# Optimization experiments

Measured on AMD Instinct MI355X. Metric: run time of the kernel, lower is better.

## Reference

```python
import jax, jax.numpy as jnp
import numpy as np

B, S, D, H = 2, 2048, 1024, 16
DK = D // H  # 64
THETA = 10000.0


def setup_inputs() -> dict:
    key = jax.random.key(0)
    ks = jax.random.split(key, 5)
    scale = 1.0 / np.sqrt(D)
    return {
        "x": jax.random.normal(ks[0], (B, S, D), dtype=jnp.float32),
        "Wq": jax.random.normal(ks[1], (D, D), dtype=jnp.float32) * scale,
        "Wk": jax.random.normal(ks[2], (D, D), dtype=jnp.float32) * scale,
        "Wv": jax.random.normal(ks[3], (D, D), dtype=jnp.float32) * scale,
        "Wo": jax.random.normal(ks[4], (D, D), dtype=jnp.float32) * scale,
    }


def _rope(t):
    # t: (B, H, S, DK); interleaved-pair rotary embedding with positions 0..S-1
    s = t.shape[-2]
    inv_freq = 1.0 / (THETA ** (jnp.arange(0, DK, 2, dtype=jnp.float32) / DK))  # (DK/2,)
    ang = jnp.arange(s, dtype=jnp.float32)[:, None] * inv_freq[None, :]  # (S, DK/2)
    cos, sin = jnp.cos(ang), jnp.sin(ang)
    x1 = t[..., 0::2]
    x2 = t[..., 1::2]
    r1 = x1 * cos - x2 * sin
    r2 = x1 * sin + x2 * cos
    return jnp.stack([r1, r2], axis=-1).reshape(t.shape)


def reference(x, Wq, Wk, Wv, Wo):
    # Projections (Linear: y = x @ W^T), split heads -> (B, H, S, DK)
    def proj(W):
        y = jnp.einsum('bsd,ed->bse', x, W)
        return y.reshape(B, S, H, DK).transpose(0, 2, 1, 3)

    Q = _rope(proj(Wq))
    K = _rope(proj(Wk))
    V = proj(Wv)

    scores = jnp.einsum('bhqd,bhkd->bhqk', Q, K)
    scores = jnp.clip(scores, -80.0, 80.0)
    causal = jnp.tril(jnp.ones((S, S), dtype=bool))  # (S, S)
    scores = jnp.where(causal, scores, -jnp.inf)
    weights = jax.nn.softmax(scores / np.sqrt(DK), axis=-1)
    att = jnp.einsum('bhqk,bhkd->bhqd', weights, V)
    att = att.transpose(0, 2, 1, 3).reshape(B, S, D)
    return jnp.einsum('bsd,ed->bse', att, Wo)
```

## Files before the change

### kernel.cpp

```cpp
#include <hip/hip_runtime.h>
#include <hip/hip_bf16.h>

#define B_  2
#define S_  2048
#define D_  1024
#define H_  16
#define DK_ 64
#define BH_ (B_*H_)
#define M_  (B_*S_)

typedef __attribute__((ext_vector_type(8))) short bf16x8;
typedef __attribute__((ext_vector_type(4))) float f32x4;

__device__ inline float bf2f(unsigned short u) {
    return __uint_as_float(((unsigned)u) << 16);
}
__device__ inline unsigned short f2bf(float f) {
    unsigned u = __float_as_uint(f);
    u += 0x7fffu + ((u >> 16) & 1u);
    return (unsigned short)(u >> 16);
}
__device__ inline unsigned short f2bf_hw(float f) {
    __hip_bfloat16 h = __float2bfloat16(f);
    return *reinterpret_cast<unsigned short*>(&h);
}
__device__ inline unsigned packbf2(float lo, float hi) {
    return (unsigned)f2bf_hw(lo) | ((unsigned)f2bf_hw(hi) << 16);
}

__device__ inline void gld16(const void* g, void* l) {
    __builtin_amdgcn_global_load_lds(
        (const __attribute__((address_space(1))) unsigned int*)g,
        (__attribute__((address_space(3))) unsigned int*)l, 16, 0, 0);
}

__global__ void cast_f32_to_bf16(const float* __restrict__ src,
                                 unsigned short* __restrict__ dst, int n) {
    int i = (blockIdx.x * blockDim.x + threadIdx.x) * 4;
    int stride = gridDim.x * blockDim.x * 4;
    for (int j = i; j < n; j += stride) {
        float4 v = *reinterpret_cast<const float4*>(src + j);
        ushort4 o;
        o.x = f2bf(v.x); o.y = f2bf(v.y); o.z = f2bf(v.z); o.w = f2bf(v.w);
        *reinterpret_cast<ushort4*>(dst + j) = o;
    }
}

__global__ void cast4_f32_to_bf16(const float* __restrict__ s0, const float* __restrict__ s1,
                                  const float* __restrict__ s2, const float* __restrict__ s3,
                                  unsigned short* __restrict__ d0, unsigned short* __restrict__ d1,
                                  unsigned short* __restrict__ d2, unsigned short* __restrict__ d3) {
    const float* s; unsigned short* d;
    switch (blockIdx.y) {
        case 0: s = s0; d = d0; break;
        case 1: s = s1; d = d1; break;
        case 2: s = s2; d = d2; break;
        default: s = s3; d = d3; break;
    }
    int j = (blockIdx.x * blockDim.x + threadIdx.x) * 4;
    float4 v = *reinterpret_cast<const float4*>(s + j);
    ushort4 o;
    o.x = f2bf(v.x); o.y = f2bf(v.y); o.z = f2bf(v.z); o.w = f2bf(v.w);
    *reinterpret_cast<ushort4*>(d + j) = o;
}

#define BM 64
#define BN 128
#define BKG 64

__global__ __launch_bounds__(256)
void gemm_qkv(const unsigned short* __restrict__ A, const unsigned short* __restrict__ Wcat,
              unsigned short* __restrict__ Qf, unsigned short* __restrict__ Kf,
              unsigned short* __restrict__ Vf) {
    __shared__ unsigned short As[BM * BKG];
    __shared__ unsigned short Bs[BN * BKG];
    const int K = D_;
    const int tid  = threadIdx.x;
    const int lane = tid & 63;
    const int wid  = tid >> 6;
    const int wm = wid & 1, wn = wid >> 1;
    const int m0 = blockIdx.y * BM, n0 = blockIdx.x * BN;
    const int g  = lane >> 4, cl = lane & 15;

    f32x4 acc[2][4];
#pragma unroll
    for (int i = 0; i < 2; i++)
#pragma unroll
        for (int j = 0; j < 4; j++) acc[i][j] = f32x4{0.f, 0.f, 0.f, 0.f};

    const int srow = tid >> 3;
    const unsigned short* Asrc[2];
    const unsigned short* Bsrc[4];
#pragma unroll
    for (int q = 0; q < 2; q++) {
        int row = srow + q * 32;
        Asrc[q] = A + (long)(m0 + row) * K + (((tid & 7) ^ (row & 7)) * 8);
    }
#pragma unroll
    for (int q = 0; q < 4; q++) {
        int row = srow + q * 32;
        Bsrc[q] = Wcat + (long)(n0 + row) * K + (((tid & 7) ^ (row & 7)) * 8);
    }

    for (int k0 = 0; k0 < K; k0 += BKG) {
        __syncthreads();
#pragma unroll
        for (int q = 0; q < 2; q++) gld16(Asrc[q] + k0, As + tid * 8 + q * 2048);
#pragma unroll
        for (int q = 0; q < 4; q++) gld16(Bsrc[q] + k0, Bs + tid * 8 + q * 2048);
        __syncthreads();

#pragma unroll
        for (int kk = 0; kk < 2; kk++) {
            bf16x8 af[2], bfr[4];
#pragma unroll
            for (int i = 0; i < 2; i++) {
                int row = wm*32 + i*16 + cl;
                af[i]  = *reinterpret_cast<const bf16x8*>(As + row * BKG + (((kk*4 + g) ^ (cl & 7)) * 8));
            }
#pragma unroll
            for (int j = 0; j < 4; j++) {
                int row = wn*64 + j*16 + cl;
                bfr[j] = *reinterpret_cast<const bf16x8*>(Bs + row * BKG + (((kk*4 + g) ^ (cl & 7)) * 8));
            }
#pragma unroll
            for (int i = 0; i < 2; i++)
#pragma unroll
                for (int j = 0; j < 4; j++)
                    acc[i][j] = __builtin_amdgcn_mfma_f32_16x16x32_bf16(af[i], bfr[j], acc[i][j], 0, 0, 0);
        }
    }

    const int mat = n0 >> 10;
    if (mat < 2) {
        unsigned short* dst = mat ? Kf : Qf;
        float invf[4];
#pragma unroll
        for (int jj = 0; jj < 4; jj++)
            invf[jj] = exp2f(-(float)(jj*8 + (cl >> 1)) * 0.4152410118569779f);
#pragma unroll
        for (int i = 0; i < 2; i++) {
#pragma unroll
            for (int jj = 0; jj < 4; jj++) {
                const int gcl = (n0 & 1023) + wn*64 + jj*16 + cl;
                const int hh = gcl >> 6;
                const int dk = jj*16 + cl;
                const int c  = dk >> 5;
                const int lsel = ((dk >> 3) & 3) << 4;
                const int e  = dk & 7;
#pragma unroll
                for (int rr = 0; rr < 4; rr++) {
                    int gr = m0 + wm*32 + i*16 + g*4 + rr;
                    int bb = gr >> 11, s = gr & (S_ - 1);
                    float v = acc[i][jj][rr];
                    float p = __shfl_xor(v, 1);
                    float ang = (float)s * invf[jj];
                    float sn = __sinf(ang), cs = __cosf(ang);
                    float r = (cl & 1) ? fmaf(v, cs, p * sn) : fmaf(v, cs, -p * sn);
                    const int lane_p = (s & 15) | lsel;
                    long idx = ((long)(bb*H_ + hh) * 128 + (s >> 4)) * 1024
                             + c * 512 + lane_p * 8 + e;
                    dst[idx] = f2bf_hw(r);
                }
            }
        }
    } else {
#pragma unroll
        for (int i = 0; i < 2; i++) {
#pragma unroll
            for (int jj = 0; jj < 4; jj++) {
                const int gcl = (n0 & 1023) + wn*64 + jj*16 + cl;
                const int hh = gcl >> 6;
                const int sbase = m0 + wm*32 + i*16 + g*4;
                const int bb = sbase >> 11, s0l = sbase & (S_ - 1);
                const int lane_p = cl | (((s0l >> 3) & 3) << 4);
                const int e0 = s0l & 7;
                ushort4 o;
                o.x = f2bf_hw(acc[i][jj][0]); o.y = f2bf_hw(acc[i][jj][1]);
                o.z = f2bf_hw(acc[i][jj][2]); o.w = f2bf_hw(acc[i][jj][3]);
                long idx = ((long)(bb*H_ + hh) * 4 + jj) * 32768
                         + (long)(s0l >> 5) * 512 + lane_p * 8 + e0;
                *reinterpret_cast<ushort4*>(Vf + idx) = o;
            }
        }
    }
}

__global__ __launch_bounds__(256)
void gemm_out(const unsigned short* __restrict__ A, const unsigned short* __restrict__ Bw,
              float* __restrict__ Cf) {
    __shared__ unsigned short As[BM * BKG];
    __shared__ unsigned short Bs[BN * BKG];
    const int K = D_;
    const int tid  = threadIdx.x;
    const int lane = tid & 63;
    const int wid  = tid >> 6;
    const int wm = wid & 1, wn = wid >> 1;
    const int m0 = blockIdx.y * BM, n0 = blockIdx.x * BN;
    const int g  = lane >> 4, cl = lane & 15;

    f32x4 acc[2][4];
#pragma unroll
    for (int i = 0; i < 2; i++)
#pragma unroll
        for (int j = 0; j < 4; j++) acc[i][j] = f32x4{0.f, 0.f, 0.f, 0.f};

    const int srow = tid >> 3;
    const unsigned short* Asrc[2];
    const unsigned short* Bsrc[4];
#pragma unroll
    for (int q = 0; q < 2; q++) {
        int row = srow + q * 32;
        Asrc[q] = A + (long)(m0 + row) * K + (((tid & 7) ^ (row & 7)) * 8);
    }
#pragma unroll
    for (int q = 0; q < 4; q++) {
        int row = srow + q * 32;
        Bsrc[q] = Bw + (long)(n0 + row) * K + (((tid & 7) ^ (row & 7)) * 8);
    }

    for (int k0 = 0; k0 < K; k0 += BKG) {
        __syncthreads();
#pragma unroll
        for (int q = 0; q < 2; q++) gld16(Asrc[q] + k0, As + tid * 8 + q * 2048);
#pragma unroll
        for (int q = 0; q < 4; q++) gld16(Bsrc[q] + k0, Bs + tid * 8 + q * 2048);
        __syncthreads();

#pragma unroll
        for (int kk = 0; kk < 2; kk++) {
            bf16x8 af[2], bfr[4];
#pragma unroll
            for (int i = 0; i < 2; i++) {
                int row = wm*32 + i*16 + cl;
                af[i]  = *reinterpret_cast<const bf16x8*>(As + row * BKG + (((kk*4 + g) ^ (cl & 7)) * 8));
            }
#pragma unroll
            for (int j = 0; j < 4; j++) {
                int row = wn*64 + j*16 + cl;
                bfr[j] = *reinterpret_cast<const bf16x8*>(Bs + row * BKG + (((kk*4 + g) ^ (cl & 7)) * 8));
            }
#pragma unroll
            for (int i = 0; i < 2; i++)
#pragma unroll
                for (int j = 0; j < 4; j++)
                    acc[i][j] = __builtin_amdgcn_mfma_f32_16x16x32_bf16(af[i], bfr[j], acc[i][j], 0, 0, 0);
        }
    }

#pragma unroll
    for (int i = 0; i < 2; i++)
#pragma unroll
        for (int j = 0; j < 4; j++)
#pragma unroll
            for (int rr = 0; rr < 4; rr++) {
                int gr = m0 + wm*32 + i*16 + g*4 + rr;
                int gc = n0 + wn*64 + j*16 + cl;
                Cf[(long)gr * D_ + gc] = acc[i][j][rr];
            }
}

#define WQ    32
#define KVBLK 64
#define LDP   72

__global__ __launch_bounds__(256)
void flash_attn(const unsigned short* __restrict__ Qf, const unsigned short* __restrict__ Kf,
                const unsigned short* __restrict__ Vf, unsigned short* __restrict__ Att) {
    __shared__ __align__(16) char smem[20480];
    const int tid  = threadIdx.x;
    const int lane = tid & 63;
    const int wid  = tid >> 6;
    const int g = lane >> 4, cl = lane & 15;
    const int bh = blockIdx.x & (BH_ - 1);
    const int pr = blockIdx.x >> 5;
    const int b = bh >> 4, h = bh & (H_ - 1);

    unsigned short* Ps = reinterpret_cast<unsigned short*>(smem) + wid * (WQ * LDP);
    f32x4* Ol = reinterpret_cast<f32x4*>(smem);
    float* Ll = reinterpret_cast<float*>(smem + 16384);

    const unsigned short* Qb = Qf + (long)bh * 131072;
    const unsigned short* Kb = Kf + (long)bh * 131072;
    const unsigned short* Vb = Vf + (long)bh * 131072;

    for (int half = 0; half < 2; half++) {
        const int qt = half ? (S_/WQ - 1 - pr) : pr;
        const int q0 = qt * WQ;
        const int nt = (q0 + WQ + KVBLK - 1) / KVBLK;

        bf16x8 aq[2][2];
#pragma unroll
        for (int m = 0; m < 2; m++)
#pragma unroll
            for (int c = 0; c < 2; c++)
                aq[m][c] = *reinterpret_cast<const bf16x8*>(Qb + ((q0 >> 4) + m) * 1024 + c * 512 + lane * 8);

        f32x4 o[2][4];
#pragma unroll
        for (int m = 0; m < 2; m++)
#pragma unroll
            for (int t = 0; t < 4; t++) o[m][t] = f32x4{0.f, 0.f, 0.f, 0.f};
        float lp[2] = {0.f, 0.f};

        for (int j = wid; j < nt; j += 4) {
            const int kv0 = j * KVBLK;
            bf16x8 bk[4][2];
#pragma unroll
            for (int n = 0; n < 4; n++)
#pragma unroll
                for (int c = 0; c < 2; c++)
                    bk[n][c] = *reinterpret_cast<const bf16x8*>(Kb + ((kv0 >> 4) + n) * 1024 + c * 512 + lane * 8);
            f32x4 sc[2][4];
#pragma unroll
            for (int m = 0; m < 2; m++)
#pragma unroll
                for (int n = 0; n < 4; n++) {
                    f32x4 z = f32x4{0.f, 0.f, 0.f, 0.f};
                    z = __builtin_amdgcn_mfma_f32_16x16x32_bf16(bk[n][0], aq[m][0], z, 0, 0, 0);
                    z = __builtin_amdgcn_mfma_f32_16x16x32_bf16(bk[n][1], aq[m][1], z, 0, 0, 0);
                    sc[m][n] = z;
                }

            if (kv0 + KVBLK - 1 > q0) {
#pragma unroll
                for (int m = 0; m < 2; m++) {
                    const int q = q0 + m*16 + cl;
#pragma unroll
                    for (int n = 0; n < 4; n++) {
                        float p4[4];
#pragma unroll
                        for (int rr = 0; rr < 4; rr++) {
                            float u = fminf(fmaf(sc[m][n][rr], 0.125f, -10.f), 0.f);
                            if (kv0 + n*16 + g*4 + rr > q) u = -1e30f;
                            p4[rr] = __expf(u);
                        }
                        lp[m] += (p4[0] + p4[1]) + (p4[2] + p4[3]);
                        *reinterpret_cast<uint2*>(Ps + (m*16 + cl) * LDP + n*16 + g*4)
                            = uint2{packbf2(p4[0], p4[1]), packbf2(p4[2], p4[3])};
                    }
                }
            } else {
#pragma unroll
                for (int m = 0; m < 2; m++) {
#pragma unroll
                    for (int n = 0; n < 4; n++) {
                        float p4[4];
#pragma unroll
                        for (int rr = 0; rr < 4; rr++)
                            p4[rr] = __expf(fminf(fmaf(sc[m][n][rr], 0.125f, -10.f), 0.f));
                        lp[m] += (p4[0] + p4[1]) + (p4[2] + p4[3]);
                        *reinterpret_cast<uint2*>(Ps + (m*16 + cl) * LDP + n*16 + g*4)
                            = uint2{packbf2(p4[0], p4[1]), packbf2(p4[2], p4[3])};
                    }
                }
            }

            bf16x8 pa[2][2];
#pragma unroll
            for (int m = 0; m < 2; m++)
#pragma unroll
                for (int c = 0; c < 2; c++)
                    pa[m][c] = *reinterpret_cast<const bf16x8*>(Ps + (m*16 + cl) * LDP + c*32 + g*8);
            bf16x8 bv[4][2];
#pragma unroll
            for (int t = 0; t < 4; t++)
#pragma unroll
                for (int c = 0; c < 2; c++)
                    bv[t][c] = *reinterpret_cast<const bf16x8*>(Vb + (long)t * 32768 + ((kv0 >> 5) + c) * 512 + lane * 8);
#pragma unroll
            for (int m = 0; m < 2; m++)
#pragma unroll
                for (int t = 0; t < 4; t++) {
                    o[m][t] = __builtin_amdgcn_mfma_f32_16x16x32_bf16(pa[m][0], bv[t][0], o[m][t], 0, 0, 0);
                    o[m][t] = __builtin_amdgcn_mfma_f32_16x16x32_bf16(pa[m][1], bv[t][1], o[m][t], 0, 0, 0);
                }
        }

        __syncthreads();
        if (wid == 1 || wid == 3) {
            const int slot = wid >> 1;
#pragma unroll
            for (int m = 0; m < 2; m++) {
#pragma unroll
                for (int t = 0; t < 4; t++)
                    Ol[(slot*8 + m*4 + t)*64 + lane] = o[m][t];
                Ll[(slot*2 + m)*64 + lane] = lp[m];
            }
        }
        __syncthreads();
        if (wid == 0 || wid == 2) {
            const int slot = wid >> 1;
#pragma unroll
            for (int m = 0; m < 2; m++) {
#pragma unroll
                for (int t = 0; t < 4; t++) {
                    f32x4 v = Ol[(slot*8 + m*4 + t)*64 + lane];
#pragma unroll
                    for (int rr = 0; rr < 4; rr++) o[m][t][rr] += v[rr];
                }
                lp[m] += Ll[(slot*2 + m)*64 + lane];
            }
        }
        __syncthreads();
        if (wid == 2) {
#pragma unroll
            for (int m = 0; m < 2; m++) {
#pragma unroll
                for (int t = 0; t < 4; t++)
                    Ol[(m*4 + t)*64 + lane] = o[m][t];
                Ll[m*64 + lane] = lp[m];
            }
        }
        __syncthreads();
        if (wid == 0) {
#pragma unroll
            for (int m = 0; m < 2; m++) {
#pragma unroll
                for (int t = 0; t < 4; t++) {
                    f32x4 v = Ol[(m*4 + t)*64 + lane];
#pragma unroll
                    for (int rr = 0; rr < 4; rr++) o[m][t][rr] += v[rr];
                }
                lp[m] += Ll[m*64 + lane];
                lp[m] += __shfl_xor(lp[m], 16);
                lp[m] += __shfl_xor(lp[m], 32);
            }
            float linv[2][4];
#pragma unroll
            for (int m = 0; m < 2; m++)
#pragma unroll
                for (int rr = 0; rr < 4; rr++)
                    linv[m][rr] = 1.0f / __shfl(lp[m], g*4 + rr);
#pragma unroll
            for (int m = 0; m < 2; m++)
#pragma unroll
                for (int t = 0; t < 4; t++)
#pragma unroll
                    for (int rr = 0; rr < 4; rr++) {
                        const int q = q0 + m*16 + g*4 + rr;
                        const int d = t*16 + cl;
                        Att[(long)(b * S_ + q) * D_ + h * DK_ + d] = f2bf_hw(o[m][t][rr] * linv[m][rr]);
                    }
        }
        __syncthreads();
    }
}

extern "C" void kernel_launch(void* const* d_in, const int* in_sizes, int n_in,
                              void* d_out, int out_size, void* d_ws, size_t ws_size,
                              hipStream_t stream) {
    const float* x  = (const float*)d_in[0];
    const float* Wq = (const float*)d_in[1];
    const float* Wk = (const float*)d_in[2];
    const float* Wv = (const float*)d_in[3];
    const float* Wo = (const float*)d_in[4];
    float* out = (float*)d_out;

    char* ws = (char*)d_ws;
    unsigned short* xb  = (unsigned short*)(ws);
    unsigned short* att = xb;
    unsigned short* WqB = (unsigned short*)(ws + (8  << 20));
    unsigned short* WkB = (unsigned short*)(ws + (10 << 20));
    unsigned short* WvB = (unsigned short*)(ws + (12 << 20));
    unsigned short* WoB = (unsigned short*)(ws + (14 << 20));
    unsigned short* Qf  = (unsigned short*)(ws + (16 << 20));
    unsigned short* Kf  = (unsigned short*)(ws + (24 << 20));
    unsigned short* Vf  = (unsigned short*)(ws + (32 << 20));

    const int nx = B_ * S_ * D_;
    cast_f32_to_bf16<<<4096, 256, 0, stream>>>(x, xb, nx);
    cast4_f32_to_bf16<<<dim3(1024, 4), 256, 0, stream>>>(Wq, Wk, Wv, Wo, WqB, WkB, WvB, WoB);

    dim3 qkvgrid(3 * D_ / BN, M_ / BM);
    gemm_qkv<<<qkvgrid, 256, 0, stream>>>(xb, WqB, Qf, Kf, Vf);

    flash_attn<<<(S_/WQ/2) * BH_, 256, 0, stream>>>(Qf, Kf, Vf, att);

    dim3 ogrid(D_ / BN, M_ / BM);
    gemm_out<<<ogrid, 256, 0, stream>>>(att, WoB, out);
}
```

Measured before the change: 115.8 us.

## Keep softmax probabilities in registers via permuted K layout; enlarge QKV GEMM tile

```diff
diff --git a/kernel.cpp b/kernel.cpp
--- a/kernel.cpp
+++ b/kernel.cpp
@@ -64,67 +64,62 @@
     *reinterpret_cast<ushort4*>(d + j) = o;
 }
 
-#define BM 64
-#define BN 128
-#define BKG 64
+#define BMQ 128
+#define BNQ 128
 
 __global__ __launch_bounds__(256)
 void gemm_qkv(const unsigned short* __restrict__ A, const unsigned short* __restrict__ Wcat,
               unsigned short* __restrict__ Qf, unsigned short* __restrict__ Kf,
               unsigned short* __restrict__ Vf) {
-    __shared__ unsigned short As[BM * BKG];
-    __shared__ unsigned short Bs[BN * BKG];
+    __shared__ unsigned short As[BMQ * 64];
+    __shared__ unsigned short Bs[BNQ * 64];
     const int K = D_;
     const int tid  = threadIdx.x;
     const int lane = tid & 63;
     const int wid  = tid >> 6;
     const int wm = wid & 1, wn = wid >> 1;
-    const int m0 = blockIdx.y * BM, n0 = blockIdx.x * BN;
+    const int m0 = blockIdx.y * BMQ, n0 = blockIdx.x * BNQ;
     const int g  = lane >> 4, cl = lane & 15;
 
-    f32x4 acc[2][4];
-#pragma unroll
-    for (int i = 0; i < 2; i++)
+    f32x4 acc[4][4];
+#pragma unroll
+    for (int i = 0; i < 4; i++)
 #pragma unroll
         for (int j = 0; j < 4; j++) acc[i][j] = f32x4{0.f, 0.f, 0.f, 0.f};
 
     const int srow = tid >> 3;
-    const unsigned short* Asrc[2];
+    const unsigned short* Asrc[4];
     const unsigned short* Bsrc[4];
-#pragma unroll
-    for (int q = 0; q < 2; q++) {
-        int row = srow + q * 32;
-        Asrc[q] = A + (long)(m0 + row) * K + (((tid & 7) ^ (row & 7)) * 8);
-    }
 #pragma unroll
     for (int q = 0; q < 4; q++) {
         int row = srow + q * 32;
-        Bsrc[q] = Wcat + (long)(n0 + row) * K + (((tid & 7) ^ (row & 7)) * 8);
-    }
-
-    for (int k0 = 0; k0 < K; k0 += BKG) {
-        __syncthreads();
-#pragma unroll
-        for (int q = 0; q < 2; q++) gld16(Asrc[q] + k0, As + tid * 8 + q * 2048);
+        Asrc[q] = A    + (long)(m0 + row) * K + (((tid & 7) ^ (srow & 7)) * 8);
+        Bsrc[q] = Wcat + (long)(n0 + row) * K + (((tid & 7) ^ (srow & 7)) * 8);
+    }
+
+    for (int k0 = 0; k0 < K; k0 += 64) {
+        __syncthreads();
+#pragma unroll
+        for (int q = 0; q < 4; q++) gld16(Asrc[q] + k0, As + tid * 8 + q * 2048);
 #pragma unroll
         for (int q = 0; q < 4; q++) gld16(Bsrc[q] + k0, Bs + tid * 8 + q * 2048);
         __syncthreads();
 
 #pragma unroll
         for (int kk = 0; kk < 2; kk++) {
-            bf16x8 af[2], bfr[4];
-#pragma unroll
-            for (int i = 0; i < 2; i++) {
-                int row = wm*32 + i*16 + cl;
-                af[i]  = *reinterpret_cast<const bf16x8*>(As + row * BKG + (((kk*4 + g) ^ (cl & 7)) * 8));
+            bf16x8 af[4], bfr[4];
+#pragma unroll
+            for (int i = 0; i < 4; i++) {
+                int row = wm*64 + i*16 + cl;
+                af[i]  = *reinterpret_cast<const bf16x8*>(As + row * 64 + (((kk*4 + g) ^ (cl & 7)) * 8));
             }
 #pragma unroll
             for (int j = 0; j < 4; j++) {
                 int row = wn*64 + j*16 + cl;
-                bfr[j] = *reinterpret_cast<const bf16x8*>(Bs + row * BKG + (((kk*4 + g) ^ (cl & 7)) * 8));
-            }
-#pragma unroll
-            for (int i = 0; i < 2; i++)
+                bfr[j] = *reinterpret_cast<const bf16x8*>(Bs + row * 64 + (((kk*4 + g) ^ (cl & 7)) * 8));
+            }
+#pragma unroll
+            for (int i = 0; i < 4; i++)
 #pragma unroll
                 for (int j = 0; j < 4; j++)
                     acc[i][j] = __builtin_amdgcn_mfma_f32_16x16x32_bf16(af[i], bfr[j], acc[i][j], 0, 0, 0);
@@ -133,45 +128,52 @@
 
     const int mat = n0 >> 10;
     if (mat < 2) {
-        unsigned short* dst = mat ? Kf : Qf;
         float invf[4];
 #pragma unroll
         for (int jj = 0; jj < 4; jj++)
             invf[jj] = exp2f(-(float)(jj*8 + (cl >> 1)) * 0.4152410118569779f);
 #pragma unroll
-        for (int i = 0; i < 2; i++) {
+        for (int i = 0; i < 4; i++) {
 #pragma unroll
             for (int jj = 0; jj < 4; jj++) {
                 const int gcl = (n0 & 1023) + wn*64 + jj*16 + cl;
                 const int hh = gcl >> 6;
                 const int dk = jj*16 + cl;
-                const int c  = dk >> 5;
-                const int lsel = ((dk >> 3) & 3) << 4;
-                const int e  = dk & 7;
 #pragma unroll
                 for (int rr = 0; rr < 4; rr++) {
-                    int gr = m0 + wm*32 + i*16 + g*4 + rr;
+                    int gr = m0 + wm*64 + i*16 + g*4 + rr;
                     int bb = gr >> 11, s = gr & (S_ - 1);
                     float v = acc[i][jj][rr];
                     float p = __shfl_xor(v, 1);
                     float ang = (float)s * invf[jj];
                     float sn = __sinf(ang), cs = __cosf(ang);
                     float r = (cl & 1) ? fmaf(v, cs, p * sn) : fmaf(v, cs, -p * sn);
-                    const int lane_p = (s & 15) | lsel;
-                    long idx = ((long)(bb*H_ + hh) * 128 + (s >> 4)) * 1024
-                             + c * 512 + lane_p * 8 + e;
-                    dst[idx] = f2bf_hw(r);
+                    long idx;
+                    if (mat == 0) {
+                        const int lane_p = (s & 15) | (((dk >> 3) & 3) << 4);
+                        idx = ((long)(bb*H_ + hh) * 128 + (s >> 4)) * 1024
+                            + (dk >> 5) * 512 + lane_p * 8 + (dk & 7);
+                        Qf[idx] = f2bf_hw(r);
+                    } else {
+                        const int vv = s & 63;
+                        const int ng = ((vv >> 5) << 1) | ((vv >> 2) & 1);
+                        const int slot = ((vv & 31) >> 3) * 4 + (vv & 3);
+                        const int lane_p = slot | (((dk >> 3) & 3) << 4);
+                        idx = (((long)(bb*H_ + hh) * 32 + (s >> 6)) * 4 + ng) * 1024
+                            + (dk >> 5) * 512 + lane_p * 8 + (dk & 7);
+                        Kf[idx] = f2bf_hw(r);
+                    }
                 }
             }
         }
     } else {
 #pragma unroll
-        for (int i = 0; i < 2; i++) {
+        for (int i = 0; i < 4; i++) {
 #pragma unroll
             for (int jj = 0; jj < 4; jj++) {
                 const int gcl = (n0 & 1023) + wn*64 + jj*16 + cl;
                 const int hh = gcl >> 6;
-                const int sbase = m0 + wm*32 + i*16 + g*4;
+                const int sbase = m0 + wm*64 + i*16 + g*4;
                 const int bb = sbase >> 11, s0l = sbase & (S_ - 1);
                 const int lane_p = cl | (((s0l >> 3) & 3) << 4);
                 const int e0 = s0l & 7;
@@ -186,11 +188,14 @@
     }
 }
 
+#define BM 64
+#define BN 128
+
 __global__ __launch_bounds__(256)
 void gemm_out(const unsigned short* __restrict__ A, const unsigned short* __restrict__ Bw,
               float* __restrict__ Cf) {
-    __shared__ unsigned short As[BM * BKG];
-    __shared__ unsigned short Bs[BN * BKG];
+    __shared__ unsigned short As[BM * 64];
+    __shared__ unsigned short Bs[BN * 64];
     const int K = D_;
     const int tid  = threadIdx.x;
     const int lane = tid & 63;
@@ -211,15 +216,15 @@
 #pragma unroll
     for (int q = 0; q < 2; q++) {
         int row = srow + q * 32;
-        Asrc[q] = A + (long)(m0 + row) * K + (((tid & 7) ^ (row & 7)) * 8);
+        Asrc[q] = A + (long)(m0 + row) * K + (((tid & 7) ^ (srow & 7)) * 8);
     }
 #pragma unroll
     for (int q = 0; q < 4; q++) {
         int row = srow + q * 32;
-        Bsrc[q] = Bw + (long)(n0 + row) * K + (((tid & 7) ^ (row & 7)) * 8);
-    }
-
-    for (int k0 = 0; k0 < K; k0 += BKG) {
+        Bsrc[q] = Bw + (long)(n0 + row) * K + (((tid & 7) ^ (srow & 7)) * 8);
+    }
+
+    for (int k0 = 0; k0 < K; k0 += 64) {
         __syncthreads();
 #pragma unroll
         for (int q = 0; q < 2; q++) gld16(Asrc[q] + k0, As + tid * 8 + q * 2048);
@@ -233,12 +238,12 @@
 #pragma unroll
             for (int i = 0; i < 2; i++) {
                 int row = wm*32 + i*16 + cl;
-                af[i]  = *reinterpret_cast<const bf16x8*>(As + row * BKG + (((kk*4 + g) ^ (cl & 7)) * 8));
+                af[i]  = *reinterpret_cast<const bf16x8*>(As + row * 64 + (((kk*4 + g) ^ (cl & 7)) * 8));
             }
 #pragma unroll
             for (int j = 0; j < 4; j++) {
                 int row = wn*64 + j*16 + cl;
-                bfr[j] = *reinterpret_cast<const bf16x8*>(Bs + row * BKG + (((kk*4 + g) ^ (cl & 7)) * 8));
+                bfr[j] = *reinterpret_cast<const bf16x8*>(Bs + row * 64 + (((kk*4 + g) ^ (cl & 7)) * 8));
             }
 #pragma unroll
             for (int i = 0; i < 2; i++)
@@ -262,12 +267,11 @@
 
 #define WQ    32
 #define KVBLK 64
-#define LDP   72
 
 __global__ __launch_bounds__(256)
 void flash_attn(const unsigned short* __restrict__ Qf, const unsigned short* __restrict__ Kf,
                 const unsigned short* __restrict__ Vf, unsigned short* __restrict__ Att) {
-    __shared__ __align__(16) char smem[20480];
+    __shared__ __align__(16) char smem[17408];
     const int tid  = threadIdx.x;
     const int lane = tid & 63;
     const int wid  = tid >> 6;
@@ -276,13 +280,15 @@
     const int pr = blockIdx.x >> 5;
     const int b = bh >> 4, h = bh & (H_ - 1);
 
-    unsigned short* Ps = reinterpret_cast<unsigned short*>(smem) + wid * (WQ * LDP);
     f32x4* Ol = reinterpret_cast<f32x4*>(smem);
     float* Ll = reinterpret_cast<float*>(smem + 16384);
 
     const unsigned short* Qb = Qf + (long)bh * 131072;
     const unsigned short* Kb = Kf + (long)bh * 131072;
     const unsigned short* Vb = Vf + (long)bh * 131072;
+
+    const float RS = 0.125f * 1.44269504f;
+    const float RB = -10.f * 1.44269504f;
 
     for (int half = 0; half < 2; half++) {
         const int qt = half ? (S_/WQ - 1 - pr) : pr;
@@ -310,7 +316,7 @@
             for (int n = 0; n < 4; n++)
 #pragma unroll
                 for (int c = 0; c < 2; c++)
-                    bk[n][c] = *reinterpret_cast<const bf16x8*>(Kb + ((kv0 >> 4) + n) * 1024 + c * 512 + lane * 8);
+                    bk[n][c] = *reinterpret_cast<const bf16x8*>(Kb + (j * 4 + n) * 1024 + c * 512 + lane * 8);
             f32x4 sc[2][4];
 #pragma unroll
             for (int m = 0; m < 2; m++)
@@ -322,59 +328,45 @@
                     sc[m][n] = z;
                 }
 
-            if (kv0 + KVBLK - 1 > q0) {
-#pragma unroll
-                for (int m = 0; m < 2; m++) {
-                    const int q = q0 + m*16 + cl;
-#pragma unroll
-                    for (int n = 0; n < 4; n++) {
-                        float p4[4];
-#pragma unroll
-                        for (int rr = 0; rr < 4; rr++) {
-                            float u = fminf(fmaf(sc[m][n][rr], 0.125f, -10.f), 0.f);
-                            if (kv0 + n*16 + g*4 + rr > q) u = -1e30f;
-                            p4[rr] = __expf(u);
-                        }
-                        lp[m] += (p4[0] + p4[1]) + (p4[2] + p4[3]);
-                        *reinterpret_cast<uint2*>(Ps + (m*16 + cl) * LDP + n*16 + g*4)
-                            = uint2{packbf2(p4[0], p4[1]), packbf2(p4[2], p4[3])};
-                    }
-                }
-            } else {
-#pragma unroll
-                for (int m = 0; m < 2; m++) {
-#pragma unroll
-                    for (int n = 0; n < 4; n++) {
-                        float p4[4];
-#pragma unroll
-                        for (int rr = 0; rr < 4; rr++)
-                            p4[rr] = __expf(fminf(fmaf(sc[m][n][rr], 0.125f, -10.f), 0.f));
-                        lp[m] += (p4[0] + p4[1]) + (p4[2] + p4[3]);
-                        *reinterpret_cast<uint2*>(Ps + (m*16 + cl) * LDP + n*16 + g*4)
-                            = uint2{packbf2(p4[0], p4[1]), packbf2(p4[2], p4[3])};
-                    }
-                }
-            }
-
-            bf16x8 pa[2][2];
-#pragma unroll
-            for (int m = 0; m < 2; m++)
-#pragma unroll
-                for (int c = 0; c < 2; c++)
-                    pa[m][c] = *reinterpret_cast<const bf16x8*>(Ps + (m*16 + cl) * LDP + c*32 + g*8);
             bf16x8 bv[4][2];
 #pragma unroll
             for (int t = 0; t < 4; t++)
 #pragma unroll
                 for (int c = 0; c < 2; c++)
                     bv[t][c] = *reinterpret_cast<const bf16x8*>(Vb + (long)t * 32768 + ((kv0 >> 5) + c) * 512 + lane * 8);
-#pragma unroll
-            for (int m = 0; m < 2; m++)
+
+            const bool diag = (kv0 + KVBLK - 1 > q0);
+#pragma unroll
+            for (int m = 0; m < 2; m++) {
+                const int q = q0 + m*16 + cl;
+                union { unsigned u[4]; bf16x8 v; } w0, w1;
+#pragma unroll
+                for (int n = 0; n < 4; n++) {
+                    float p4[4];
+#pragma unroll
+                    for (int rr = 0; rr < 4; rr++) {
+                        float u2 = fminf(fmaf(sc[m][n][rr], RS, RB), 0.f);
+                        float pe = __builtin_amdgcn_exp2f(u2);
+                        if (diag) {
+                            const int kv = kv0 + ((n >> 1) << 5) + (g << 3) + ((n & 1) << 2) + rr;
+                            if (kv > q) pe = 0.f;
+                        }
+                        p4[rr] = pe;
+                    }
+                    lp[m] += (p4[0] + p4[1]) + (p4[2] + p4[3]);
+                    const unsigned lo = packbf2(p4[0], p4[1]);
+                    const unsigned hi = packbf2(p4[2], p4[3]);
+                    if (n == 0)      { w0.u[0] = lo; w0.u[1] = hi; }
+                    else if (n == 1) { w0.u[2] = lo; w0.u[3] = hi; }
+                    else if (n == 2) { w1.u[0] = lo; w1.u[1] = hi; }
+                    else             { w1.u[2] = lo; w1.u[3] = hi; }
+                }
 #pragma unroll
                 for (int t = 0; t < 4; t++) {
-                    o[m][t] = __builtin_amdgcn_mfma_f32_16x16x32_bf16(pa[m][0], bv[t][0], o[m][t], 0, 0, 0);
-                    o[m][t] = __builtin_amdgcn_mfma_f32_16x16x32_bf16(pa[m][1], bv[t][1], o[m][t], 0, 0, 0);
-                }
+                    o[m][t] = __builtin_amdgcn_mfma_f32_16x16x32_bf16(w0.v, bv[t][0], o[m][t], 0, 0, 0);
+                    o[m][t] = __builtin_amdgcn_mfma_f32_16x16x32_bf16(w1.v, bv[t][1], o[m][t], 0, 0, 0);
+                }
+            }
         }
 
         __syncthreads();
@@ -472,7 +464,7 @@
     cast_f32_to_bf16<<<4096, 256, 0, stream>>>(x, xb, nx);
     cast4_f32_to_bf16<<<dim3(1024, 4), 256, 0, stream>>>(Wq, Wk, Wv, Wo, WqB, WkB, WvB, WoB);
 
-    dim3 qkvgrid(3 * D_ / BN, M_ / BM);
+    dim3 qkvgrid(3 * D_ / BNQ, M_ / BMQ);
     gemm_qkv<<<qkvgrid, 256, 0, stream>>>(xb, WqB, Qf, Kf, Vf);
 
     flash_attn<<<(S_/WQ/2) * BH_, 256, 0, stream>>>(Qf, Kf, Vf, att);
```

Result: no change. 117.2 us (+1.2%).
